# Kernel tuning notes

Hardware: AMD Instinct MI355X
Metric: run time of the kernel (lower is better)

Reference implementation:

```python
import jax, jax.numpy as jnp
import numpy as np

NUM_NODES = 256
IN_FEAT = 64
HIDDEN = 512
N_CLASSES = 2
BATCH = 256


def setup_inputs() -> dict:
    key = jax.random.key(0)
    ks = jax.random.split(key, 10)
    return {
        "z": jax.random.normal(ks[0], (BATCH, 1, NUM_NODES, NUM_NODES), dtype=jnp.float32),
        "node_emb": jax.random.normal(ks[1], (NUM_NODES, IN_FEAT), dtype=jnp.float32),
        "w1": jax.random.normal(ks[2], (IN_FEAT, HIDDEN), dtype=jnp.float32) * (1.0 / np.sqrt(IN_FEAT)),
        "b1": jnp.zeros((HIDDEN,), dtype=jnp.float32),
        "w2": jax.random.normal(ks[3], (HIDDEN, HIDDEN), dtype=jnp.float32) * (1.0 / np.sqrt(HIDDEN)),
        "b2": jnp.zeros((HIDDEN,), dtype=jnp.float32),
        "w3": jax.random.normal(ks[4], (HIDDEN, HIDDEN), dtype=jnp.float32) * (1.0 / np.sqrt(HIDDEN)),
        "b3": jnp.zeros((HIDDEN,), dtype=jnp.float32),
        "fcw": jax.random.normal(ks[5], (HIDDEN, N_CLASSES), dtype=jnp.float32) * (1.0 / np.sqrt(HIDDEN)),
        "fcb": jnp.zeros((N_CLASSES,), dtype=jnp.float32),
    }


def reference(z, node_emb, w1, b1, w2, b2, w3, b3, fcw, fcb):
    # z: (B, 1, N, N) latent interpreted as weighted adjacency
    z_sq = jnp.squeeze(z, axis=1)                         # (B, N, N)
    A = jax.nn.sigmoid(z_sq)
    A = (A + jnp.swapaxes(A, 1, 2)) * 0.5                  # symmetrize
    A_hat = A + jnp.eye(A.shape[-1], dtype=A.dtype)[None]  # add self loops
    D_hat = jnp.sum(A_hat, axis=2) + 1e-6                  # (B, N) degrees
    d_inv_sqrt = D_hat ** -0.5
    # norm_A = D^{-1/2} A_hat D^{-1/2} via row/col scaling (same math as diag bmm)
    norm_A = A_hat * d_inv_sqrt[:, :, None] * d_inv_sqrt[:, None, :]

    X = jnp.broadcast_to(node_emb[None], (z.shape[0],) + node_emb.shape)  # (B, N, F)
    H1 = jax.nn.relu(jnp.einsum('bij,bjh->bih', norm_A, X @ w1 + b1))
    H2 = jax.nn.relu(jnp.einsum('bij,bjh->bih', norm_A, H1 @ w2 + b2))
    H3 = jax.nn.relu(jnp.einsum('bij,bjh->bih', norm_A, H2 @ w3 + b3))
    graph_emb = jnp.mean(H3, axis=1)                       # (B, H)
    logits = graph_emb @ fcw + fcb                         # (B, n_classes)
    return logits
```

## Files before the change

kernel.cpp:

```cpp
#include <hip/hip_runtime.h>
#include <stdint.h>

#define B_ 256
#define N_ 256
#define F_ 64
#define H_ 512

typedef _Float16 f16;
typedef _Float16 f16x8 __attribute__((ext_vector_type(8)));
typedef _Float16 f16x4 __attribute__((ext_vector_type(4)));
typedef _Float16 f16x2 __attribute__((ext_vector_type(2)));
typedef float    f32x4 __attribute__((ext_vector_type(4)));

__device__ __forceinline__ float sigmoidf_(float x) {
    return 1.0f / (1.0f + __expf(-x));
}

__global__ __launch_bounds__(512) void k_fsum(const float* __restrict__ z,
                                              f16* __restrict__ nA) {
    constexpr int LD = 258;
    __shared__ f16 T[256 * LD];
    __shared__ float cpart[8][256];
    __shared__ float rbuf[256];
    __shared__ float Dv[256];

    const int b = blockIdx.x;
    const int tid = threadIdx.x, lane = tid & 63, w = tid >> 6;
    const float* zb = z + (size_t)b * (N_ * N_);

    float colacc[4] = {0.f, 0.f, 0.f, 0.f};
    for (int r = 0; r < 32; r++) {
        int i = w * 32 + r;
        float4 v = *(const float4*)(zb + (size_t)i * N_ + lane * 4);
        float s0 = sigmoidf_(v.x), s1 = sigmoidf_(v.y),
              s2 = sigmoidf_(v.z), s3 = sigmoidf_(v.w);
        f16x2 p0 = { (f16)s0, (f16)s1 }, p1 = { (f16)s2, (f16)s3 };
        *(f16x2*)&T[i * LD + lane * 4]     = p0;
        *(f16x2*)&T[i * LD + lane * 4 + 2] = p1;
        colacc[0] += s0; colacc[1] += s1; colacc[2] += s2; colacc[3] += s3;
        float rs = s0 + s1 + s2 + s3;
        for (int off = 32; off; off >>= 1) rs += __shfl_down(rs, off, 64);
        if (lane == 0) rbuf[i] = rs;
    }
    #pragma unroll
    for (int k = 0; k < 4; k++) cpart[w][lane * 4 + k] = colacc[k];
    __syncthreads();

    if (tid < 256) {
        float cs = 0.f;
        #pragma unroll
        for (int ww = 0; ww < 8; ww++) cs += cpart[ww][tid];
        Dv[tid] = rsqrtf(1.0f + 1e-6f + 0.5f * (rbuf[tid] + cs));
    }
    __syncthreads();

    const int j8 = (tid & 31) * 8;
    float dj[8];
    #pragma unroll
    for (int k = 0; k < 8; k++) dj[k] = Dv[j8 + k];
    f16* Ob = nA + (size_t)b * (N_ * N_);
    for (int it = 0; it < 16; it++) {
        int i = it * 16 + (tid >> 5);
        float di = Dv[i];
        f16x2 dd[4];
        #pragma unroll
        for (int c = 0; c < 4; c++)
            dd[c] = *(const f16x2*)&T[i * LD + j8 + c * 2];
        f16x8 o;
        #pragma unroll
        for (int k = 0; k < 8; k++) {
            float sij = (float)dd[k >> 1][k & 1];
            float v = 0.5f * (sij + (float)T[(j8 + k) * LD + i]);
            if (i == j8 + k) v += 1.0f;
            o[k] = (f16)(v * di * dj[k]);
        }
        *(f16x8*)&Ob[(size_t)i * N_ + j8] = o;
    }
}

__global__ __launch_bounds__(256) void k_prep(const float* __restrict__ ne,
                                              const float* __restrict__ w1,
                                              const float* __restrict__ b1,
                                              const float* __restrict__ w2,
                                              const float* __restrict__ w3,
                                              f16* __restrict__ XW1t,
                                              f16* __restrict__ w2t,
                                              f16* __restrict__ w3t) {
    int bid = blockIdx.x;
    if (bid < 512) {
        int h = bid, node = threadIdx.x;
        float s = b1[h];
        #pragma unroll 8
        for (int k = 0; k < F_; k++) s += ne[node * F_ + k] * w1[k * H_ + h];
        XW1t[h * N_ + node] = (f16)s;
    } else {
        int idx4 = bid - 512;
        int which = idx4 >> 10;
        const float* src = which ? w3 : w2;
        f16* dst = which ? w3t : w2t;
        int idx = (idx4 & 1023) * 256 + threadIdx.x;
        int k = idx >> 9, n = idx & 511;
        dst[n * H_ + k] = (f16)src[k * H_ + n];
    }
}

template <int KDIM, int MODE>
__global__ __launch_bounds__(256, 4) void k_gemm(const f16* __restrict__ A, long aBatch,
                                                 const f16* __restrict__ Bt, long bBatch,
                                                 f16* __restrict__ Out,
                                                 const float* __restrict__ bias,
                                                 float* __restrict__ gp) {
    __shared__ f16 As[128 * 64];
    __shared__ f16 Bs[128 * 64];
    const int tid  = threadIdx.x;
    const int lane = tid & 63, wave = tid >> 6;
    const int wm = wave >> 1, wn = wave & 1;

    const int lin = blockIdx.x;
    const int xcd = lin & 7, q = lin >> 3;
    const int n_t = q & 3, p = q >> 2;
    const int grp = xcd * 64 + p;
    const int b   = grp >> 1, m_t = grp & 1;
    const int m0 = m_t * 128, n0 = n_t * 128;

    const f16* Ab = A + (size_t)b * aBatch;
    const f16* Bb = Bt + (size_t)b * bBatch;

    f32x4 acc[4][4];
    #pragma unroll
    for (int i = 0; i < 4; i++)
        #pragma unroll
        for (int j = 0; j < 4; j++)
            #pragma unroll
            for (int r = 0; r < 4; r++) acc[i][j][r] = 0.0f;

    const int lr = lane >> 3;
    const int kc = (lane & 7) ^ lr;

    const int ln15 = lane & 15;

    for (int kk = 0; kk < KDIM; kk += 64) {
        #pragma unroll
        for (int c = 0; c < 4; c++) {
            int chunk = wave * 4 + c;
            int row = chunk * 8 + lr;
            __builtin_amdgcn_global_load_lds(
                (__attribute__((address_space(1))) void*)(Ab + (size_t)(m0 + row) * KDIM + kk + kc * 8),
                (__attribute__((address_space(3))) void*)(&As[chunk * 512]), 16, 0, 0);
            __builtin_amdgcn_global_load_lds(
                (__attribute__((address_space(1))) void*)(Bb + (size_t)(n0 + row) * KDIM + kk + kc * 8),
                (__attribute__((address_space(3))) void*)(&Bs[chunk * 512]), 16, 0, 0);
        }
        __syncthreads();

        #pragma unroll
        for (int ks = 0; ks < 2; ks++) {
            const int rkc = ks * 4 + (lane >> 4);
            f16x8 aF[4];
            #pragma unroll
            for (int t = 0; t < 4; t++) {
                int ra = wm * 64 + t * 16 + ln15;
                aF[t] = *(const f16x8*)&As[(ra * 8 + (rkc ^ (ra & 7))) * 8];
            }
            #pragma unroll
            for (int h2 = 0; h2 < 2; h2++) {
                f16x8 bF[2];
                #pragma unroll
                for (int t = 0; t < 2; t++) {
                    int rb = wn * 64 + (h2 * 2 + t) * 16 + ln15;
                    bF[t] = *(const f16x8*)&Bs[(rb * 8 + (rkc ^ (rb & 7))) * 8];
                }
                #pragma unroll
                for (int mt = 0; mt < 4; mt++)
                    #pragma unroll
                    for (int t = 0; t < 2; t++)
                        acc[mt][h2 * 2 + t] = __builtin_amdgcn_mfma_f32_16x16x32_f16(aF[mt], bF[t], acc[mt][h2 * 2 + t], 0, 0, 0);
            }
        }
        __syncthreads();
    }

    const int quad = lane >> 4;
    if (MODE == 0) {
        f16* Ob = Out + (size_t)b * (N_ * H_);
        #pragma unroll
        for (int mt = 0; mt < 4; mt++) {
            int node = m0 + wm * 64 + mt * 16 + quad * 4;
            #pragma unroll
            for (int nt = 0; nt < 4; nt++) {
                int h = n0 + wn * 64 + nt * 16 + ln15;
                #pragma unroll
                for (int rr = 0; rr < 4; rr++) {
                    float v = acc[mt][nt][rr];
                    v = v > 0.f ? v : 0.f;
                    Ob[(size_t)(node + rr) * H_ + h] = (f16)v;
                }
            }
        }
    }
}

template <int REDUCE>
__global__ __launch_bounds__(512, 2) void k_fused(const f16* __restrict__ Hin,
                                                  const f16* __restrict__ Wt,
                                                  const float* __restrict__ bias,
                                                  const f16* __restrict__ nA,
                                                  f16* __restrict__ Hout,
                                                  float* __restrict__ gp) {
    __shared__ f16 As[2][16384];
    __shared__ f16 WU[32768];

    const int tid  = threadIdx.x;
    const int lane = tid & 63, wave = tid >> 6;
    const int ln15 = lane & 15, quad = lane >> 4;
    const int wm = wave >> 1, wn = wave & 1;

    const int lin = blockIdx.x;
    const int xcd = lin & 7, p = lin >> 3;
    const int grp = xcd * 128 + p;
    const int b = grp >> 2, hc = grp & 3;

    const f16* Hb = Hin + (size_t)b * (N_ * H_);
    const f16* Ab = nA + (size_t)b * (N_ * N_);
    const f16* Wc = Wt + (size_t)(hc * 128) * H_;

    const int lr = lane >> 3;
    const int kc = (lane & 7) ^ lr;

    auto stage1 = [&](int buf, int kt) {
        #pragma unroll
        for (int c = 0; c < 4; c++) {
            int chunk = wave * 4 + c;
            int row = chunk * 8 + lr;
            __builtin_amdgcn_global_load_lds(
                (__attribute__((address_space(1))) void*)(Hb + (size_t)row * H_ + kt * 64 + kc * 8),
                (__attribute__((address_space(3))) void*)(&As[buf][chunk * 512]), 16, 0, 0);
        }
        #pragma unroll
        for (int c = 0; c < 2; c++) {
            int chunk = wave * 2 + c;
            int row = chunk * 8 + lr;
            __builtin_amdgcn_global_load_lds(
                (__attribute__((address_space(1))) void*)(Wc + (size_t)row * H_ + kt * 64 + kc * 8),
                (__attribute__((address_space(3))) void*)(&WU[buf * 8192 + chunk * 512]), 16, 0, 0);
        }
    };
    auto stage2 = [&](int buf, int jt) {
        #pragma unroll
        for (int c = 0; c < 4; c++) {
            int chunk = wave * 4 + c;
            int row = chunk * 8 + lr;
            __builtin_amdgcn_global_load_lds(
                (__attribute__((address_space(1))) void*)(Ab + (size_t)row * N_ + jt * 64 + kc * 8),
                (__attribute__((address_space(3))) void*)(&As[buf][chunk * 512]), 16, 0, 0);
        }
    };

    f32x4 acc[4][4];
    #pragma unroll
    for (int i = 0; i < 4; i++)
        #pragma unroll
        for (int j = 0; j < 4; j++)
            #pragma unroll
            for (int r = 0; r < 4; r++) acc[i][j][r] = 0.0f;

    stage1(0, 0);
    __syncthreads();
    for (int kt = 0; kt < 8; ++kt) {
        if (kt < 7) stage1((kt + 1) & 1, kt + 1);
        else        stage2(0, 0);
        const int buf = kt & 1;
        #pragma unroll
        for (int ks = 0; ks < 2; ks++) {
            const int rkc = ks * 4 + quad;
            f16x8 aF[4], bF[4];
            #pragma unroll
            for (int t = 0; t < 4; t++) {
                int ra = wm * 64 + t * 16 + ln15;
                aF[t] = *(const f16x8*)&As[buf][(ra * 8 + (rkc ^ (ra & 7))) * 8];
            }
            #pragma unroll
            for (int t = 0; t < 4; t++) {
                int rb = wn * 64 + t * 16 + ln15;
                bF[t] = *(const f16x8*)&WU[buf * 8192 + (rb * 8 + (rkc ^ (rb & 7))) * 8];
            }
            #pragma unroll
            for (int mt = 0; mt < 4; mt++)
                #pragma unroll
                for (int nt = 0; nt < 4; nt++)
                    acc[mt][nt] = __builtin_amdgcn_mfma_f32_16x16x32_f16(aF[mt], bF[nt], acc[mt][nt], 0, 0, 0);
        }
        __syncthreads();
    }

    #pragma unroll
    for (int nt = 0; nt < 4; nt++) {
        int hl = wn * 64 + nt * 16 + ln15;
        float bv = bias[hc * 128 + hl];
        #pragma unroll
        for (int mt = 0; mt < 4; mt++) {
            int j = wm * 64 + mt * 16 + quad * 4;
            int slot = (j >> 3) ^ (hl & 7);
            f16x4 v;
            #pragma unroll
            for (int rr = 0; rr < 4; rr++) v[rr] = (f16)(acc[mt][nt][rr] + bv);
            *(f16x4*)&WU[hl * 256 + slot * 8 + (j & 7)] = v;
        }
    }
    __syncthreads();

    #pragma unroll
    for (int i = 0; i < 4; i++)
        #pragma unroll
        for (int j = 0; j < 4; j++)
            #pragma unroll
            for (int r = 0; r < 4; r++) acc[i][j][r] = 0.0f;

    for (int jt = 0; jt < 4; ++jt) {
        if (jt < 3) stage2((jt + 1) & 1, jt + 1);
        const int buf = jt & 1;
        #pragma unroll
        for (int ks = 0; ks < 2; ks++) {
            const int rkc = ks * 4 + quad;
            f16x8 aF[4], bF[4];
            #pragma unroll
            for (int t = 0; t < 4; t++) {
                int ra = wm * 64 + t * 16 + ln15;
                aF[t] = *(const f16x8*)&As[buf][(ra * 8 + (rkc ^ (ra & 7))) * 8];
            }
            #pragma unroll
            for (int t = 0; t < 4; t++) {
                int rb = wn * 64 + t * 16 + ln15;
                int g = jt * 8 + rkc;
                bF[t] = *(const f16x8*)&WU[rb * 256 + ((g ^ (rb & 7)) * 8)];
            }
            #pragma unroll
            for (int mt = 0; mt < 4; mt++)
                #pragma unroll
                for (int nt = 0; nt < 4; nt++)
                    acc[mt][nt] = __builtin_amdgcn_mfma_f32_16x16x32_f16(aF[mt], bF[nt], acc[mt][nt], 0, 0, 0);
        }
        __syncthreads();
    }

    if (REDUCE == 0) {
        f16* Ob = Hout + (size_t)b * (N_ * H_);
        #pragma unroll
        for (int mt = 0; mt < 4; mt++) {
            int node = wm * 64 + mt * 16 + quad * 4;
            #pragma unroll
            for (int nt = 0; nt < 4; nt++) {
                int hg = hc * 128 + wn * 64 + nt * 16 + ln15;
                #pragma unroll
                for (int rr = 0; rr < 4; rr++) {
                    float v = acc[mt][nt][rr];
                    v = v > 0.f ? v : 0.f;
                    Ob[(size_t)(node + rr) * H_ + hg] = (f16)v;
                }
            }
        }
    } else {
        float part[4];
        #pragma unroll
        for (int nt = 0; nt < 4; nt++) {
            float s = 0.f;
            #pragma unroll
            for (int mt = 0; mt < 4; mt++)
                #pragma unroll
                for (int rr = 0; rr < 4; rr++) {
                    float v = acc[mt][nt][rr];
                    s += (v > 0.f ? v : 0.f);
                }
            s += __shfl_down(s, 32, 64);
            s += __shfl_down(s, 16, 64);
            part[nt] = s;
        }
        __syncthreads();
        float* red = (float*)&As[0][0];
        if (quad == 0) {
            #pragma unroll
            for (int nt = 0; nt < 4; nt++)
                red[wave * 64 + nt * 16 + ln15] = part[nt];
        }
        __syncthreads();
        if (tid < 128) {
            int wnl = tid >> 6, cl = tid & 63;
            float g = red[(0 * 2 + wnl) * 64 + cl] + red[(1 * 2 + wnl) * 64 + cl]
                    + red[(2 * 2 + wnl) * 64 + cl] + red[(3 * 2 + wnl) * 64 + cl];
            gp[(size_t)b * H_ + hc * 128 + tid] = g;
        }
    }
}

__global__ __launch_bounds__(256) void k_logits(const float* __restrict__ gp,
                                                const float* __restrict__ fcw,
                                                const float* __restrict__ fcb,
                                                float* __restrict__ out) {
    int b = blockIdx.x, tid = threadIdx.x;
    const float* g = gp + (size_t)b * H_;
    float g0 = g[tid];
    float g1 = g[tid + 256];
    float p0 = g0 * fcw[tid * 2 + 0] + g1 * fcw[(tid + 256) * 2 + 0];
    float p1 = g0 * fcw[tid * 2 + 1] + g1 * fcw[(tid + 256) * 2 + 1];
    for (int off = 32; off; off >>= 1) {
        p0 += __shfl_down(p0, off, 64);
        p1 += __shfl_down(p1, off, 64);
    }
    __shared__ float r0[4], r1[4];
    int lane = tid & 63, w = tid >> 6;
    if (lane == 0) { r0[w] = p0; r1[w] = p1; }
    __syncthreads();
    const float inv = 1.0f / N_;
    if (tid == 0) out[b * 2 + 0] = (r0[0] + r0[1] + r0[2] + r0[3]) * inv + fcb[0];
    if (tid == 1) out[b * 2 + 1] = (r1[0] + r1[1] + r1[2] + r1[3]) * inv + fcb[1];
}

extern "C" void kernel_launch(void* const* d_in, const int* in_sizes, int n_in,
                              void* d_out, int out_size, void* d_ws, size_t ws_size,
                              hipStream_t stream) {
    const float* z   = (const float*)d_in[0];
    const float* ne  = (const float*)d_in[1];
    const float* w1  = (const float*)d_in[2];
    const float* b1  = (const float*)d_in[3];
    const float* w2  = (const float*)d_in[4];
    const float* b2  = (const float*)d_in[5];
    const float* w3  = (const float*)d_in[6];
    const float* b3  = (const float*)d_in[7];
    const float* fcw = (const float*)d_in[8];
    const float* fcb = (const float*)d_in[9];
    float* out = (float*)d_out;

    char* ws = (char*)d_ws;
    f16*   T     = (f16*)(ws + 0);
    f16*   nA    = (f16*)(ws + 67108864);
    f16*   Hh    = (f16*)(ws + 100663296);
    float* gpart = (float*)(ws + 100663296);
    f16*   XW1t  = (f16*)(ws + 167772160);
    f16*   w2t   = (f16*)(ws + 168034304);
    f16*   w3t   = (f16*)(ws + 168558592);

    k_fsum<<<256, 512, 0, stream>>>(z, nA);
    k_prep<<<2560, 256, 0, stream>>>(ne, w1, b1, w2, w3, XW1t, w2t, w3t);

    k_gemm<256, 0><<<2048, 256, 0, stream>>>(nA, 65536, XW1t, 0, Hh, nullptr, nullptr);
    k_fused<0><<<1024, 512, 0, stream>>>(Hh, w2t, b2, nA, T, nullptr);
    k_fused<1><<<1024, 512, 0, stream>>>(T, w3t, b3, nA, nullptr, gpart);

    k_logits<<<B_, 256, 0, stream>>>(gpart, fcw, fcb, out);
}
```

Baseline: 315.1 us.

## Load weight and adjacency fragments directly to registers with hand-scheduled pipeline

Weight tiles in the first GEMM and normalized-adjacency tiles in the second GEMM are now fetched straight from global memory into VGPR double buffers with inline-asm dwordx4 loads, instead of going through LDS. Only the H tile stays staged in LDS. Both loops are fully unrolled with explicit vmcnt waits, raw s_barrier, sched_barrier and setprio around the MFMA bursts. The aim is to cut LDS traffic and barrier stalls and to overlap loads with MFMA work, at the cost of much higher register pressure and fragile hand-counted waitcnt values.

```diff
diff --git a/kernel.cpp b/kernel.cpp
--- a/kernel.cpp
+++ b/kernel.cpp
@@ -15,6 +15,18 @@
 __device__ __forceinline__ float sigmoidf_(float x) {
     return 1.0f / (1.0f + __expf(-x));
 }
+
+#define BAR_ACQ(N) do { \
+    asm volatile("s_waitcnt vmcnt(" #N ")" ::: "memory"); \
+    __builtin_amdgcn_s_barrier(); \
+    __builtin_amdgcn_sched_barrier(0); } while (0)
+#define BAR_REL() do { \
+    __builtin_amdgcn_sched_barrier(0); \
+    __builtin_amdgcn_s_barrier(); } while (0)
+
+#define GLOADX4(dst, ptr, IMM) \
+    asm volatile("global_load_dwordx4 %0, %1, off offset:" #IMM \
+                 : "=v"(dst) : "v"(ptr) : "memory")
 
 __global__ __launch_bounds__(512) void k_fsum(const float* __restrict__ z,
                                               f16* __restrict__ nA) {
@@ -227,7 +239,7 @@
     const int lr = lane >> 3;
     const int kc = (lane & 7) ^ lr;
 
-    auto stage1 = [&](int buf, int kt) {
+    auto stageA = [&](int buf, int kt) {
         #pragma unroll
         for (int c = 0; c < 4; c++) {
             int chunk = wave * 4 + c;
@@ -236,25 +248,30 @@
                 (__attribute__((address_space(1))) void*)(Hb + (size_t)row * H_ + kt * 64 + kc * 8),
                 (__attribute__((address_space(3))) void*)(&As[buf][chunk * 512]), 16, 0, 0);
         }
-        #pragma unroll
-        for (int c = 0; c < 2; c++) {
-            int chunk = wave * 2 + c;
-            int row = chunk * 8 + lr;
-            __builtin_amdgcn_global_load_lds(
-                (__attribute__((address_space(1))) void*)(Wc + (size_t)row * H_ + kt * 64 + kc * 8),
-                (__attribute__((address_space(3))) void*)(&WU[buf * 8192 + chunk * 512]), 16, 0, 0);
-        }
     };
-    auto stage2 = [&](int buf, int jt) {
-        #pragma unroll
-        for (int c = 0; c < 4; c++) {
-            int chunk = wave * 4 + c;
-            int row = chunk * 8 + lr;
-            __builtin_amdgcn_global_load_lds(
-                (__attribute__((address_space(1))) void*)(Ab + (size_t)row * N_ + jt * 64 + kc * 8),
-                (__attribute__((address_space(3))) void*)(&As[buf][chunk * 512]), 16, 0, 0);
-        }
-    };
+
+    const f16* wbase[4];
+    const f16* abase[4];
+    #pragma unroll
+    for (int t = 0; t < 4; t++) {
+        wbase[t] = Wc + (size_t)(wn * 64 + t * 16 + ln15) * H_ + quad * 8;
+        abase[t] = Ab + (size_t)(wm * 64 + t * 16 + ln15) * N_ + quad * 8;
+    }
+
+#define LOADW(DST, KT) do { \
+    _Pragma("unroll") \
+    for (int t_ = 0; t_ < 4; t_++) { \
+        const f16* p_ = wbase[t_] + (KT) * 64; \
+        GLOADX4(DST[t_], p_, 0); \
+        GLOADX4(DST[4 + t_], p_, 64); \
+    } } while (0)
+#define LOADA2(DST, JT) do { \
+    _Pragma("unroll") \
+    for (int t_ = 0; t_ < 4; t_++) { \
+        const f16* p_ = abase[t_] + (JT) * 64; \
+        GLOADX4(DST[t_], p_, 0); \
+        GLOADX4(DST[4 + t_], p_, 64); \
+    } } while (0)
 
     f32x4 acc[4][4];
     #pragma unroll
@@ -264,34 +281,57 @@
             #pragma unroll
             for (int r = 0; r < 4; r++) acc[i][j][r] = 0.0f;
 
-    stage1(0, 0);
-    __syncthreads();
-    for (int kt = 0; kt < 8; ++kt) {
-        if (kt < 7) stage1((kt + 1) & 1, kt + 1);
-        else        stage2(0, 0);
-        const int buf = kt & 1;
-        #pragma unroll
-        for (int ks = 0; ks < 2; ks++) {
-            const int rkc = ks * 4 + quad;
-            f16x8 aF[4], bF[4];
-            #pragma unroll
-            for (int t = 0; t < 4; t++) {
-                int ra = wm * 64 + t * 16 + ln15;
-                aF[t] = *(const f16x8*)&As[buf][(ra * 8 + (rkc ^ (ra & 7))) * 8];
-            }
-            #pragma unroll
-            for (int t = 0; t < 4; t++) {
-                int rb = wn * 64 + t * 16 + ln15;
-                bF[t] = *(const f16x8*)&WU[buf * 8192 + (rb * 8 + (rkc ^ (rb & 7))) * 8];
-            }
-            #pragma unroll
-            for (int mt = 0; mt < 4; mt++)
-                #pragma unroll
-                for (int nt = 0; nt < 4; nt++)
-                    acc[mt][nt] = __builtin_amdgcn_mfma_f32_16x16x32_f16(aF[mt], bF[nt], acc[mt][nt], 0, 0, 0);
-        }
-        __syncthreads();
-    }
+#define S1_STEP(ASBUF, W_) do { \
+    __builtin_amdgcn_s_setprio(1); \
+    _Pragma("unroll") \
+    for (int ks = 0; ks < 2; ks++) { \
+        const int rkc = ks * 4 + quad; \
+        f16x8 aF[4]; \
+        _Pragma("unroll") \
+        for (int t_ = 0; t_ < 4; t_++) { \
+            int ra = wm * 64 + t_ * 16 + ln15; \
+            aF[t_] = *(const f16x8*)&(ASBUF)[(ra * 8 + (rkc ^ (ra & 7))) * 8]; \
+        } \
+        _Pragma("unroll") \
+        for (int mt = 0; mt < 4; mt++) \
+            _Pragma("unroll") \
+            for (int nt = 0; nt < 4; nt++) \
+                acc[mt][nt] = __builtin_amdgcn_mfma_f32_16x16x32_f16(aF[mt], W_[ks * 4 + nt], acc[mt][nt], 0, 0, 0); \
+    } \
+    __builtin_amdgcn_s_setprio(0); } while (0)
+
+#define S2_STEP(JT, AN_) do { \
+    __builtin_amdgcn_s_setprio(1); \
+    _Pragma("unroll") \
+    for (int ks = 0; ks < 2; ks++) { \
+        const int rkc = ks * 4 + quad; \
+        f16x8 bF[4]; \
+        _Pragma("unroll") \
+        for (int t_ = 0; t_ < 4; t_++) { \
+            int rb = wn * 64 + t_ * 16 + ln15; \
+            int g = (JT) * 8 + rkc; \
+            bF[t_] = *(const f16x8*)&WU[rb * 256 + ((g ^ (rb & 7)) * 8)]; \
+        } \
+        _Pragma("unroll") \
+        for (int mt = 0; mt < 4; mt++) \
+            _Pragma("unroll") \
+            for (int nt = 0; nt < 4; nt++) \
+                acc[mt][nt] = __builtin_amdgcn_mfma_f32_16x16x32_f16(AN_[ks * 4 + mt], bF[nt], acc[mt][nt], 0, 0, 0); \
+    } \
+    __builtin_amdgcn_s_setprio(0); } while (0)
+
+    f16x8 wA[8], wB[8];
+    f16x8 nAa[8], nAb[8];
+
+    stageA(0, 0); LOADW(wA, 0);
+    stageA(1, 1); LOADW(wB, 1); BAR_ACQ(12); S1_STEP(As[0], wA); BAR_REL();
+    stageA(0, 2); LOADW(wA, 2); BAR_ACQ(12); S1_STEP(As[1], wB); BAR_REL();
+    stageA(1, 3); LOADW(wB, 3); BAR_ACQ(12); S1_STEP(As[0], wA); BAR_REL();
+    stageA(0, 4); LOADW(wA, 4); BAR_ACQ(12); S1_STEP(As[1], wB); BAR_REL();
+    stageA(1, 5); LOADW(wB, 5); BAR_ACQ(12); S1_STEP(As[0], wA); BAR_REL();
+    stageA(0, 6); LOADW(wA, 6); BAR_ACQ(12); S1_STEP(As[1], wB); BAR_REL();
+    stageA(1, 7); LOADW(wB, 7); BAR_ACQ(12); S1_STEP(As[0], wA); BAR_REL();
+    LOADA2(nAa, 0);             BAR_ACQ(8);  S1_STEP(As[1], wB); BAR_REL();
 
     #pragma unroll
     for (int nt = 0; nt < 4; nt++) {
@@ -307,7 +347,9 @@
             *(f16x4*)&WU[hl * 256 + slot * 8 + (j & 7)] = v;
         }
     }
-    __syncthreads();
+    asm volatile("s_waitcnt lgkmcnt(0)" ::: "memory");
+    __builtin_amdgcn_s_barrier();
+    __builtin_amdgcn_sched_barrier(0);
 
     #pragma unroll
     for (int i = 0; i < 4; i++)
@@ -316,32 +358,10 @@
             #pragma unroll
             for (int r = 0; r < 4; r++) acc[i][j][r] = 0.0f;
 
-    for (int jt = 0; jt < 4; ++jt) {
-        if (jt < 3) stage2((jt + 1) & 1, jt + 1);
-        const int buf = jt & 1;
-        #pragma unroll
-        for (int ks = 0; ks < 2; ks++) {
-            const int rkc = ks * 4 + quad;
-            f16x8 aF[4], bF[4];
-            #pragma unroll
-            for (int t = 0; t < 4; t++) {
-                int ra = wm * 64 + t * 16 + ln15;
-                aF[t] = *(const f16x8*)&As[buf][(ra * 8 + (rkc ^ (ra & 7))) * 8];
-            }
-            #pragma unroll
-            for (int t = 0; t < 4; t++) {
-                int rb = wn * 64 + t * 16 + ln15;
-                int g = jt * 8 + rkc;
-                bF[t] = *(const f16x8*)&WU[rb * 256 + ((g ^ (rb & 7)) * 8)];
-            }
-            #pragma unroll
-            for (int mt = 0; mt < 4; mt++)
-                #pragma unroll
-                for (int nt = 0; nt < 4; nt++)
-                    acc[mt][nt] = __builtin_amdgcn_mfma_f32_16x16x32_f16(aF[mt], bF[nt], acc[mt][nt], 0, 0, 0);
-        }
-        __syncthreads();
-    }
+    LOADA2(nAb, 1); BAR_ACQ(8); S2_STEP(0, nAa); BAR_REL();
+    LOADA2(nAa, 2); BAR_ACQ(8); S2_STEP(1, nAb); BAR_REL();
+    LOADA2(nAb, 3); BAR_ACQ(8); S2_STEP(2, nAa); BAR_REL();
+                    BAR_ACQ(0); S2_STEP(3, nAb); BAR_REL();
 
     if (REDUCE == 0) {
         f16* Ob = Hout + (size_t)b * (N_ * H_);
@@ -390,6 +410,10 @@
             gp[(size_t)b * H_ + hc * 128 + tid] = g;
         }
     }
+#undef LOADW
+#undef LOADA2
+#undef S1_STEP
+#undef S2_STEP
 }
 
 __global__ __launch_bounds__(256) void k_logits(const float* __restrict__ gp,
```

Measured after the change: 421.3 us. 1.34x slower.
